# Kernel optimization log

Hardware: AMD Instinct MI355X
Metric: run time of the kernel (lower is better)

The kernel has to match this reference:

```python
import jax, jax.numpy as jnp
import numpy as np

B = 128
IN = 256
NLVL = 6
KLVL = 3
CH = 4
C = 4 * CH * CH          # 64 channels per node
OU = 8                   # out_filter_siz_u
OV = 8                   # out_filter_siz_v
NK = 2 ** KLVL           # 8 leaf nodes per axis
W_SCALE = 1.0 / 16.0     # ~1/sqrt(2*2*C) so 7 stacked relu-convs stay numerically sane


def setup_inputs() -> dict:
    key = jax.random.key(0)
    ks = jax.random.split(key, 2 * NLVL + 4)
    fx = IN // 2 ** NLVL  # 4: input patch filter size
    inp = {}
    inp["in_data"] = jax.random.normal(ks[0], (B, IN, IN, 1), jnp.float32)
    inp["in_filter"] = jax.random.normal(ks[1], (fx, fx, 1, C), jnp.float32) * W_SCALE
    inp["in_bias"] = jnp.zeros((C,), jnp.float32)
    i = 2
    for lvl in range(1, NLVL + 1):
        n = 2 ** min(lvl, KLVL)  # node grid: grows to 2^klvl then stays
        inp[f"f{lvl}"] = jax.random.normal(ks[i], (n, n, 2, 2, C, C), jnp.float32) * W_SCALE
        inp[f"b{lvl}"] = jnp.zeros((n, n, C), jnp.float32)
        i += 1
    inp["Wd"] = jax.random.normal(ks[i], (NK, NK, 2, C, OU * OV), jnp.float32) * W_SCALE
    return inp


def _node_conv(x, w, b):
    # x: [Nu,Nv,B,H,W,C]; w: [Nu,Nv,2,2,C,C]; 2x2 stride-2 VALID conv per node
    Nu, Nv, Bn, H, W, Cc = x.shape
    xr = x.reshape(Nu, Nv, Bn, H // 2, 2, W // 2, 2, Cc)
    y = jnp.einsum('uvbhxwyc,uvxyco->uvbhwo', xr, w)
    return jax.nn.relu(y + b[:, :, None, None, None, :])


def _forward(in_data, in_filter, in_bias, fs, bs, Wd):
    Bn = in_data.shape[0]
    fx, fy = in_filter.shape[0], in_filter.shape[1]
    # input interp conv: stride == kernel -> non-overlapping patch GEMM
    xr = in_data[..., 0].reshape(Bn, in_data.shape[1] // fx, fx, in_data.shape[2] // fy, fy)
    x = jax.nn.relu(jnp.einsum('bxpyq,pqc->bxyc', xr, in_filter[:, :, 0, :]) + in_bias)
    x = x[None, None]  # [1,1,B,2^nlvl,2^nlvl,C] node grid
    for lvl in range(1, NLVL + 1):
        if lvl <= KLVL:
            # children (itu,itv) read parent (itu//2, itv//2)
            x = jnp.repeat(jnp.repeat(x, 2, axis=0), 2, axis=1)
        x = _node_conv(x, fs[lvl - 1], bs[lvl - 1])
    feats = x[:, :, :, 0, 0, :]  # [NK,NK,B,C]; spatial is 1x1 at level nlvl
    out = jnp.einsum('uvbc,uvrck->uvbrk', feats, Wd)  # r in {real, imag}
    out = out.reshape(NK, NK, Bn, 2, OU, OV)
    out = jnp.transpose(out, (2, 0, 4, 1, 5, 3))  # [B,itu,ou,itv,ov,2]
    return out.reshape(Bn, NK * OU, NK * OV, 2)


def reference(in_data, in_filter, in_bias, f1, b1, f2, b2, f3, b3, f4, b4, f5, b5, f6, b6, Wd):
    fs = (f1, f2, f3, f4, f5, f6)
    bs = (b1, b2, b3, b4, b5, b6)
    return _forward(in_data, in_filter, in_bias, fs, bs, Wd)
```

## Files before the change

### kernel.cpp

```cpp
#include <hip/hip_runtime.h>
#include <hip/hip_bf16.h>
#include <cstdint>
#include <cstddef>


typedef __attribute__((ext_vector_type(8))) short short8;
typedef __attribute__((ext_vector_type(4))) float f32x4;
typedef unsigned short ushort_t;

static __device__ __forceinline__ float b2f(const __hip_bfloat16 x) {
    return __bfloat162float(x);
}
static __device__ __forceinline__ ushort_t f2bf(float x) {
    __hip_bfloat16 h = __float2bfloat16(x);
    ushort_t u;
    __builtin_memcpy(&u, &h, 2);
    return u;
}
static __device__ __forceinline__ void gl_lds16(const void* g, void* l) {
    __builtin_amdgcn_global_load_lds(
        (const __attribute__((address_space(1))) void*)g,
        (__attribute__((address_space(3))) void*)l, 16, 0, 0);
}
#define WAIT_LGKM0() __builtin_amdgcn_s_waitcnt(0xC07F)
#define WAIT_VM0()   __builtin_amdgcn_s_waitcnt(0x0F70)

#define PREP_BLOCKS 2533

static __device__ __forceinline__ void prep_work(
    int gid, int isbf,
    const void* f1, const void* f2, const void* f3,
    const void* f4, const void* f5, const void* f6, const void* wdsrc,
    const void* b1, const void* b2, const void* b3,
    const void* b4, const void* b5, const void* b6,
    ushort_t* __restrict__ wbuf, ushort_t* __restrict__ wdbuf,
    float* __restrict__ bbuf)
{
    if (gid >= 648448) return;
    if (gid >= 630784) {
        const int bg = gid - 630784;
        const void* src; int base;
        if      (bg <   256) { src = b1; base = 0;     }
        else if (bg <  1280) { src = b2; base = 256;   }
        else if (bg <  5376) { src = b3; base = 1280;  }
        else if (bg <  9472) { src = b4; base = 5376;  }
        else if (bg < 13568) { src = b5; base = 9472;  }
        else                 { src = b6; base = 13568; }
        const int local = bg - base;
        bbuf[bg] = isbf ? b2f(((const __hip_bfloat16*)src)[local])
                        : ((const float*)src)[local];
        return;
    }
    if (gid >= 565248) {
        const int local = gid - 565248;
        const int lane = local & 63;
        const int slot = (local >> 6) & 15;
        const int site = local >> 10;
        const int ks2 = slot >> 3, nh = slot & 7, q = lane >> 4;
        const int n = nh * 16 + (lane & 15);
        const int r = n >> 6, kk = n & 63;
        const int cbase = ks2 * 32 + q * 8;
        ushort_t pk[8];
        if (isbf) {
            const ushort_t* s = (const ushort_t*)wdsrc;
            #pragma unroll
            for (int j = 0; j < 8; j++)
                pk[j] = s[(((size_t)(site * 2 + r) * 64 + cbase + j) * 64) + kk];
        } else {
            const float* s = (const float*)wdsrc;
            #pragma unroll
            for (int j = 0; j < 8; j++)
                pk[j] = f2bf(s[(((size_t)(site * 2 + r) * 64 + cbase + j) * 64) + kk]);
        }
        *(uint4*)&wdbuf[(size_t)local * 8] = *(uint4*)pk;
        return;
    }
    const void* fsrc; int base;
    if      (gid <   8192) { fsrc = f1; base = 0;      }
    else if (gid <  40960) { fsrc = f2; base = 8192;   }
    else if (gid < 172032) { fsrc = f3; base = 40960;  }
    else if (gid < 303104) { fsrc = f4; base = 172032; }
    else if (gid < 434176) { fsrc = f5; base = 303104; }
    else                   { fsrc = f6; base = 434176; }
    const int local = gid - base;
    const int lane = local & 63;
    const int slot = (local >> 6) & 7;
    const int sitetap = local >> 9;
    const int ks = slot >> 2, nh = slot & 3, q = lane >> 4;
    const int n = (lane & 15) + nh * 16;
    const int kbase = ks * 32 + q * 8;
    ushort_t pk[8];
    if (isbf) {
        const ushort_t* s = (const ushort_t*)fsrc + (size_t)sitetap * 4096;
        #pragma unroll
        for (int j = 0; j < 8; j++) pk[j] = s[(kbase + j) * 64 + n];
    } else {
        const float* s = (const float*)fsrc + (size_t)sitetap * 4096;
        #pragma unroll
        for (int j = 0; j < 8; j++) pk[j] = f2bf(s[(kbase + j) * 64 + n]);
    }
    *(uint4*)&wbuf[(size_t)gid * 8] = *(uint4*)pk;
}

static __device__ __forceinline__ void stage0_body(
    int blk, int isbf,
    const void* __restrict__ in_data, const void* __restrict__ filt,
    const void* __restrict__ bias, __hip_bfloat16* __restrict__ x0,
    int b_off, int Bc)
{
    const int X  = blk & 63;
    const int bl = blk >> 6;
    const int bg = bl + b_off;

    __shared__ float sIn[4][256];
    __shared__ float sF[16][64];
    __shared__ float sB[64];

    const int t = threadIdx.x;
    const size_t srow = ((size_t)bg * 256 + (size_t)X * 4) * 256;

    if (isbf) {
        const __hip_bfloat16* src = (const __hip_bfloat16*)in_data + srow;
        #pragma unroll
        for (int i = 0; i < 4; i++) {
            int flat = i * 256 + t;
            int p = flat >> 8, col = flat & 255;
            sIn[p][col] = b2f(src[(size_t)p * 256 + col]);
        }
        const __hip_bfloat16* fsrc = (const __hip_bfloat16*)filt;
        #pragma unroll
        for (int i = 0; i < 4; i++) {
            int flat = i * 256 + t;
            sF[flat >> 6][flat & 63] = b2f(fsrc[flat]);
        }
        if (t < 64) sB[t] = b2f(((const __hip_bfloat16*)bias)[t]);
    } else {
        const float* src = (const float*)in_data + srow;
        const int p = t >> 6, c4 = (t & 63) * 4;
        *(float4*)&sIn[p][c4] = *(const float4*)(src + (size_t)p * 256 + c4);
        const float* fsrc = (const float*)filt;
        #pragma unroll
        for (int i = 0; i < 4; i++) {
            int flat = i * 256 + t;
            sF[flat >> 6][flat & 63] = fsrc[flat];
        }
        if (t < 64) sB[t] = ((const float*)bias)[t];
    }
    __syncthreads();

    const int ty = t >> 4;
    const int tc = t & 15;

    float acc[4][4];
    {
        const float4 bv = *(const float4*)&sB[tc * 4];
        #pragma unroll
        for (int yi = 0; yi < 4; yi++) {
            acc[yi][0] = bv.x; acc[yi][1] = bv.y;
            acc[yi][2] = bv.z; acc[yi][3] = bv.w;
        }
    }

    #pragma unroll
    for (int p = 0; p < 4; p++) {
        float4 rin[4], rf[4];
        #pragma unroll
        for (int yi = 0; yi < 4; yi++)
            rin[yi] = *(const float4*)&sIn[p][ty * 16 + yi * 4];
        #pragma unroll
        for (int q = 0; q < 4; q++)
            rf[q] = *(const float4*)&sF[p * 4 + q][tc * 4];
        #pragma unroll
        for (int yi = 0; yi < 4; yi++) {
            #pragma unroll
            for (int q = 0; q < 4; q++) {
                const float a = ((const float*)&rin[yi])[q];
                acc[yi][0] = fmaf(a, rf[q].x, acc[yi][0]);
                acc[yi][1] = fmaf(a, rf[q].y, acc[yi][1]);
                acc[yi][2] = fmaf(a, rf[q].z, acc[yi][2]);
                acc[yi][3] = fmaf(a, rf[q].w, acc[yi][3]);
            }
        }
    }

    ushort_t* dst = (ushort_t*)x0;
    #pragma unroll
    for (int yi = 0; yi < 4; yi++) {
        uint2 pk;
        pk.x = (uint32_t)f2bf(fmaxf(acc[yi][0], 0.f))
             | ((uint32_t)f2bf(fmaxf(acc[yi][1], 0.f)) << 16);
        pk.y = (uint32_t)f2bf(fmaxf(acc[yi][2], 0.f))
             | ((uint32_t)f2bf(fmaxf(acc[yi][3], 0.f)) << 16);
        const int wpos = ty * 4 + yi;
        *(uint2*)(dst + ((size_t)(X * 64 + wpos) * Bc + bl) * 64 + tc * 4) = pk;
    }
}

__global__ __launch_bounds__(256) void k_prep0(
    const void* __restrict__ in_data,
    const void* f1, const void* f2, const void* f3,
    const void* f4, const void* f5, const void* f6, const void* wdsrc,
    const void* b1, const void* b2, const void* b3,
    const void* b4, const void* b5, const void* b6,
    ushort_t* __restrict__ wbuf, ushort_t* __restrict__ wdbuf,
    float* __restrict__ bbuf, int* __restrict__ flag,
    const void* __restrict__ filt, const void* __restrict__ bias0,
    __hip_bfloat16* __restrict__ x0, int Bc)
{
    __shared__ int sflag;
    const int t = threadIdx.x;
    if (t < 64) {
        const float v = __uint_as_float(((const uint32_t*)in_data)[t]);
        const bool plaus = (v == 0.0f) || (fabsf(v) > 1e-8f && fabsf(v) < 1e4f);
        const unsigned long long m = __ballot(plaus);
        if (t == 0) sflag = (__popcll(m) >= 48) ? 0 : 1;
    }
    __syncthreads();
    const int isbf = sflag;

    if (blockIdx.x < PREP_BLOCKS) {
        if (blockIdx.x == 0 && t == 0) *flag = isbf;
        prep_work(blockIdx.x * 256 + t, isbf,
                  f1, f2, f3, f4, f5, f6, wdsrc,
                  b1, b2, b3, b4, b5, b6, wbuf, wdbuf, bbuf);
    } else {
        stage0_body(blockIdx.x - PREP_BLOCKS, isbf, in_data, filt, bias0, x0, 0, Bc);
    }
}

__global__ __launch_bounds__(256) void k_stage0(
    const void* __restrict__ in_data, const void* __restrict__ filt,
    const void* __restrict__ bias, __hip_bfloat16* __restrict__ x0,
    const int* __restrict__ flag, int b_off, int Bc)
{
    stage0_body(blockIdx.x, *flag, in_data, filt, bias, x0, b_off, Bc);
}

__global__ __launch_bounds__(256) void k_level4(
    const __hip_bfloat16* __restrict__ xin,
    const ushort_t* __restrict__ wbuf,
    const float* __restrict__ bbuf,
    __hip_bfloat16* __restrict__ xout,
    int Nv_out, int HW, int Bc, int mtiles)
{
    __shared__ ushort_t smem[20480];
    __shared__ float sBias[4][64];
    ushort_t* sA = smem;
    ushort_t* sB = smem + 4096;

    int idx = blockIdx.x;
    const int mt = idx % mtiles; idx /= mtiles;
    const int w  = idx % HW; idx /= HW;
    const int h  = idx % HW; idx /= HW;
    const int Nv_in = Nv_out >> 1;
    const int vp = idx % Nv_in;
    const int up = idx / Nv_in;

    const int t = threadIdx.x;
    const int wave = t >> 6, lane = t & 63;
    const int lm = lane & 15, lq = lane >> 4;

    {
        const int ct = t >> 6, o = t & 63;
        const int so_t = (2 * up + (ct >> 1)) * Nv_out + (2 * vp + (ct & 1));
        sBias[ct][o] = bbuf[so_t * 64 + o];
    }

    const int so = (2 * up + (wave >> 1)) * Nv_out + (2 * vp + (wave & 1));
    const int H_in = HW * 2;
    const size_t pstride = (size_t)Bc * 64;
    const size_t siteb = (size_t)(up * Nv_in + vp) * H_in * H_in * pstride;
    const ushort_t* wsite = wbuf + (size_t)so * 4 * 4096;

    const f32x4 zero = {0.f, 0.f, 0.f, 0.f};
    f32x4 acc[4][4];
    #pragma unroll
    for (int i = 0; i < 4; i++)
        #pragma unroll
        for (int j = 0; j < 4; j++) acc[i][j] = zero;

    for (int tap = 0; tap < 4; tap++) {
        const int hi = 2 * h + (tap >> 1), wi = 2 * w + (tap & 1);
        const size_t tapoff = siteb + ((size_t)hi * H_in + wi) * pstride;
        #pragma unroll
        for (int s2 = 0; s2 < 2; s2++) {
            const int s = wave * 2 + s2;
            const int ks = s >> 2, mh = s & 3;
            int b = mt * 64 + lm + mh * 16;
            if (b >= Bc) b = Bc - 1;
            gl_lds16(xin + tapoff + (size_t)b * 64 + ks * 32 + lq * 8,
                     &sA[s * 512]);
        }
        const ushort_t* wt = wsite + (size_t)tap * 4096;
        #pragma unroll
        for (int s = 0; s < 8; s++) {
            gl_lds16(wt + s * 512 + lane * 8, &sB[wave * 4096 + s * 512]);
        }
        __syncthreads();

        #pragma unroll
        for (int ks = 0; ks < 2; ks++) {
            short8 bf0 = *(const short8*)&sB[wave * 4096 + (ks * 4 + 0) * 512 + lane * 8];
            short8 bf1 = *(const short8*)&sB[wave * 4096 + (ks * 4 + 1) * 512 + lane * 8];
            short8 bf2 = *(const short8*)&sB[wave * 4096 + (ks * 4 + 2) * 512 + lane * 8];
            short8 bf3 = *(const short8*)&sB[wave * 4096 + (ks * 4 + 3) * 512 + lane * 8];
            #pragma unroll
            for (int fm = 0; fm < 4; fm++) {
                short8 a = *(const short8*)&sA[(ks * 4 + fm) * 512 + lane * 8];
                acc[fm][0] = __builtin_amdgcn_mfma_f32_16x16x32_bf16(a, bf0, acc[fm][0], 0, 0, 0);
                acc[fm][1] = __builtin_amdgcn_mfma_f32_16x16x32_bf16(a, bf1, acc[fm][1], 0, 0, 0);
                acc[fm][2] = __builtin_amdgcn_mfma_f32_16x16x32_bf16(a, bf2, acc[fm][2], 0, 0, 0);
                acc[fm][3] = __builtin_amdgcn_mfma_f32_16x16x32_bf16(a, bf3, acc[fm][3], 0, 0, 0);
            }
        }
        __syncthreads();
    }

    float bv[4];
    #pragma unroll
    for (int fn = 0; fn < 4; fn++) bv[fn] = sBias[wave][fn * 16 + lm];
    ushort_t* so_buf = smem + wave * 4352;
    #pragma unroll
    for (int fm = 0; fm < 4; fm++) {
        #pragma unroll
        for (int fn = 0; fn < 4; fn++) {
            #pragma unroll
            for (int r = 0; r < 4; r++) {
                const int row = fm * 16 + lq * 4 + r;
                so_buf[row * 68 + fn * 16 + lm] =
                    f2bf(fmaxf(acc[fm][fn][r] + bv[fn], 0.f));
            }
        }
    }
    __syncthreads();

    const size_t obase = ((size_t)so * HW * HW + (size_t)h * HW + w) * pstride;
    #pragma unroll
    for (int i = 0; i < 8; i++) {
        const int task = i * 64 + lane;
        const int oct = task & 7, row = task >> 3;
        const int b = mt * 64 + row;
        if (b < Bc) {
            *(uint4*)(xout + obase + (size_t)b * 64 + oct * 8) =
                *(const uint4*)&so_buf[row * 68 + oct * 8];
        }
    }
}

__global__ __launch_bounds__(256) void k_f456(
    const __hip_bfloat16* __restrict__ xin,
    const ushort_t* __restrict__ w4, const ushort_t* __restrict__ w5,
    const ushort_t* __restrict__ w6, const ushort_t* __restrict__ wd,
    const float* __restrict__ b4, const float* __restrict__ b5,
    const float* __restrict__ b6,
    void* __restrict__ out, const int* __restrict__ flag,
    int Bc, int b_off, int mtiles)
{
    const int isbf = *flag;
    const int bx = blockIdx.x;
    const int mt = bx % mtiles;
    const int site = bx / mtiles;
    const int u = site >> 3, v = site & 7;

    __shared__ ushort_t smem[37376];

    const int t = threadIdx.x;
    const int wv = t >> 6, lane = t & 63;
    const int lm = lane & 15, lq = lane >> 4;

    const ushort_t* w6s = w6 + (size_t)site * 16384 + lane * 8;
    const ushort_t* wds = wd + (size_t)site * 8192  + lane * 8;

    float bv4[4], bv5[4];
    #pragma unroll
    for (int fn = 0; fn < 4; fn++) {
        bv4[fn] = b4[site * 64 + fn * 16 + lm];
        bv5[fn] = b5[site * 64 + fn * 16 + lm];
    }
    const float bv6 = b6[site * 64 + wv * 16 + lm];

    {
        const ushort_t* w4s = w4 + (size_t)site * 16384;
        #pragma unroll
        for (int s2 = 0; s2 < 8; s2++) {
            const int s = wv * 8 + s2;
            gl_lds16(w4s + s * 512 + lane * 8, &smem[s * 512]);
        }
    }
    __syncthreads();

    const f32x4 zero = {0.f, 0.f, 0.f, 0.f};
    const int h5 = wv >> 1, w5p = wv & 1;
    ushort_t* mid1w = smem + 16384 + wv * 4224;
    ushort_t* Aw = smem + 33280 + wv * 1024;
    const size_t pstride = (size_t)Bc * 64;

    int brow = mt * 16 + lm;
    if (brow >= Bc) brow = Bc - 1;
    const __hip_bfloat16* xbase =
        xin + (size_t)site * 64 * pstride + (size_t)brow * 64 + lq * 8;

    for (int i = 0; i < 4; i++) {
        const int h4 = 2 * h5 + (i >> 1), w4p = 2 * w5p + (i & 1);
        f32x4 acc[4];
        #pragma unroll
        for (int b_ = 0; b_ < 4; b_++) acc[b_] = zero;

        for (int tap = 0; tap < 4; tap++) {
            const int h3 = 2 * h4 + (tap >> 1), w3 = 2 * w4p + (tap & 1);
            const size_t poff = (size_t)(h3 * 8 + w3) * pstride;
            WAIT_LGKM0();
            #pragma unroll
            for (int ks = 0; ks < 2; ks++) {
                gl_lds16(xbase + poff + ks * 32, &Aw[ks * 512]);
            }
            WAIT_VM0();
            __builtin_amdgcn_sched_barrier(0);
            #pragma unroll
            for (int ks = 0; ks < 2; ks++) {
                short8 a = *(const short8*)&Aw[ks * 512 + lane * 8];
                #pragma unroll
                for (int fn = 0; fn < 4; fn++) {
                    short8 bfr = *(const short8*)&smem[(tap * 8 + ks * 4 + fn) * 512 + lane * 8];
                    acc[fn] = __builtin_amdgcn_mfma_f32_16x16x32_bf16(a, bfr, acc[fn], 0, 0, 0);
                }
            }
        }
        #pragma unroll
        for (int fn = 0; fn < 4; fn++) {
            #pragma unroll
            for (int r = 0; r < 4; r++) {
                const int m = lq * 4 + r;
                const int ch = fn * 16 + lm;
                mid1w[m * 264 + i * 64 + ch] =
                    f2bf(fmaxf(acc[fn][r] + bv4[fn], 0.f));
            }
        }
    }
    __syncthreads();

    {
        const ushort_t* w5s = w5 + (size_t)site * 16384;
        #pragma unroll
        for (int s2 = 0; s2 < 8; s2++) {
            const int s = wv * 8 + s2;
            gl_lds16(w5s + s * 512 + lane * 8, &smem[s * 512]);
        }
    }
    __syncthreads();

    short8 b3r[8];
    short8 wdr[4];
    {
        f32x4 acc2[4];
        #pragma unroll
        for (int b_ = 0; b_ < 4; b_++) acc2[b_] = zero;

        #pragma unroll
        for (int i = 0; i < 4; i++) {
            #pragma unroll
            for (int ks = 0; ks < 2; ks++) {
                short8 a0 = *(const short8*)&mid1w[lm * 264 + i * 64 + ks * 32 + lq * 8];
                #pragma unroll
                for (int fn = 0; fn < 4; fn++) {
                    short8 bfr = *(const short8*)&smem[(i * 8 + ks * 4 + fn) * 512 + lane * 8];
                    acc2[fn] = __builtin_amdgcn_mfma_f32_16x16x32_bf16(a0, bfr, acc2[fn], 0, 0, 0);
                }
            }
        }

        #pragma unroll
        for (int tap = 0; tap < 4; tap++)
            #pragma unroll
            for (int ks = 0; ks < 2; ks++)
                b3r[tap * 2 + ks] = *(const short8*)(w6s + (tap * 8 + ks * 4 + wv) * 512);
        #pragma unroll
        for (int ks = 0; ks < 2; ks++)
            #pragma unroll
            for (int n2 = 0; n2 < 2; n2++)
                wdr[ks * 2 + n2] = *(const short8*)(wds + (ks * 8 + 2 * wv + n2) * 512);

        #pragma unroll
        for (int fn = 0; fn < 4; fn++) {
            #pragma unroll
            for (int r = 0; r < 4; r++) {
                const int m = lq * 4 + r;
                const int ch = fn * 16 + lm;
                mid1w[m * 72 + ch] =
                    f2bf(fmaxf(acc2[fn][r] + bv5[fn], 0.f));
            }
        }
    }
    __syncthreads();

    {
        f32x4 acc3 = zero;
        #pragma unroll
        for (int tap = 0; tap < 4; tap++) {
            const ushort_t* sl = smem + 16384 + tap * 4224;
            #pragma unroll
            for (int ks = 0; ks < 2; ks++) {
                short8 a0 = *(const short8*)&sl[lm * 72 + ks * 32 + lq * 8];
                acc3 = __builtin_amdgcn_mfma_f32_16x16x32_bf16(a0, b3r[tap * 2 + ks], acc3, 0, 0, 0);
            }
        }
        ushort_t* mid3 = smem + 33280;
        #pragma unroll
        for (int r = 0; r < 4; r++) {
            const int m = lq * 4 + r;
            const int ch = wv * 16 + lm;
            mid3[m * 72 + ch] = f2bf(fmaxf(acc3[r] + bv6, 0.f));
        }
    }
    __syncthreads();

    {
        const ushort_t* mid3 = smem + 33280;
        f32x4 acc4[2];
        acc4[0] = zero; acc4[1] = zero;
        #pragma unroll
        for (int ks = 0; ks < 2; ks++) {
            short8 a0 = *(const short8*)&mid3[lm * 72 + ks * 32 + lq * 8];
            #pragma unroll
            for (int n2 = 0; n2 < 2; n2++) {
                acc4[n2] = __builtin_amdgcn_mfma_f32_16x16x32_bf16(a0, wdr[ks * 2 + n2], acc4[n2], 0, 0, 0);
            }
        }
        #pragma unroll
        for (int n2 = 0; n2 < 2; n2++) {
            const int n = (2 * wv + n2) * 16 + lm;
            const int rr = n >> 6, ou = (n >> 3) & 7, ov = n & 7;
            const size_t obase =
                (((size_t)(u * 8 + ou)) * 64 + (v * 8 + ov)) * 2 + rr;
            #pragma unroll
            for (int reg = 0; reg < 4; reg++) {
                const int brw = mt * 16 + lq * 4 + reg;
                if (brw < Bc) {
                    const size_t oidx = obase + (size_t)(b_off + brw) * 8192;
                    if (isbf) ((__hip_bfloat16*)out)[oidx] =
                        __float2bfloat16(acc4[n2][reg]);
                    else ((float*)out)[oidx] = acc4[n2][reg];
                }
            }
        }
    }
}

extern "C" void kernel_launch(void* const* d_in, const int* in_sizes, int n_in,
                              void* d_out, int out_size, void* d_ws, size_t ws_size,
                              hipStream_t stream)
{
    (void)in_sizes; (void)n_in; (void)out_size;

    const void* in_data = d_in[0];
    const void* filt    = d_in[1];
    const void* bias0   = d_in[2];
    const void* fl[7];
    const void* bl[7];
    for (int l = 1; l <= 6; l++) {
        fl[l] = d_in[1 + 2 * l];
        bl[l] = d_in[2 + 2 * l];
    }
    const void* Wd = d_in[15];

    const int Bfull = 128;
    const size_t perB = (size_t)64 * 64 * 64;

    const size_t wbufBytes  = 565248ull * 16;
    const size_t wdbufBytes = 65536ull * 16;
    const size_t bbufBytes  = 17664ull * 4;
    const size_t headBytes  = 256 + wbufBytes + wdbufBytes + bbufBytes;

    const size_t avail = ws_size > headBytes ? ws_size - headBytes : 0;
    int Bc = 0;
    for (int c = 128; c >= 1; c >>= 1) {
        if ((size_t)2 * c * perB * sizeof(__hip_bfloat16) <= avail) { Bc = c; break; }
    }
    if (Bc == 0) return;

    int* flag = (int*)d_ws;
    ushort_t* wbuf  = (ushort_t*)((char*)d_ws + 256);
    ushort_t* wdbuf = (ushort_t*)((char*)d_ws + 256 + wbufBytes);
    float* bbuf = (float*)((char*)d_ws + 256 + wbufBytes + wdbufBytes);
    __hip_bfloat16* bufA = (__hip_bfloat16*)((char*)d_ws + headBytes);
    __hip_bfloat16* bufB = bufA + (size_t)Bc * perB;

    static const size_t w_off[7] = {0, 0, 65536, 327680, 1376256, 2424832, 3473408};
    static const int    b_off_tab[7] = {0, 0, 256, 1280, 5376, 9472, 13568};

    const int mt4 = (Bc + 63) / 64;
    const int mt16 = (Bc + 15) / 16;

    for (int b_off = 0; b_off < Bfull; b_off += Bc) {
        if (b_off == 0) {
            k_prep0<<<dim3(PREP_BLOCKS + Bc * 64), 256, 0, stream>>>(
                in_data,
                fl[1], fl[2], fl[3], fl[4], fl[5], fl[6], Wd,
                bl[1], bl[2], bl[3], bl[4], bl[5], bl[6],
                wbuf, wdbuf, bbuf, flag,
                filt, bias0, bufA, Bc);
        } else {
            k_stage0<<<dim3(Bc * 64), 256, 0, stream>>>(in_data, filt, bias0, bufA, flag, b_off, Bc);
        }

        __hip_bfloat16* cur = bufA;
        __hip_bfloat16* nxt = bufB;
        for (int lvl = 1; lvl <= 3; lvl++) {
            const int Nu = 1 << lvl;
            const int H  = 64 >> lvl;
            const int Nv_in = Nu >> 1;
            dim3 grid(Nv_in * Nv_in * H * H * mt4);
            k_level4<<<grid, 256, 0, stream>>>(cur, wbuf + w_off[lvl],
                bbuf + b_off_tab[lvl], nxt, Nu, H, Bc, mt4);
            __hip_bfloat16* tmp = cur; cur = nxt; nxt = tmp;
        }

        k_f456<<<dim3(64 * mt16), 256, 0, stream>>>(cur,
            wbuf + w_off[4], wbuf + w_off[5], wbuf + w_off[6], wdbuf,
            bbuf + b_off_tab[4], bbuf + b_off_tab[5], bbuf + b_off_tab[6],
            d_out, flag, Bc, b_off, mt16);
    }
}
```

Measured before the change: 249.0 us.

## Prefetch all level-4 taps at once and hold weights in registers

The level-4 node-conv kernel now issues every activation load for all four taps to LDS up front, one tap per wave, instead of running a load/sync/compute loop per tap. Each wave's weights (32 short8 fragments) go straight from global memory into registers, skipping the LDS weight staging and the bias shared-memory table. This cuts the per-tap barriers and the serialised load latency, and it shrinks LDS use, with a launch bound of 2 blocks per CU. In exchange it needs many more vector registers (128 VGPRs for weights plus accumulators), which could force spills or lower occupancy.

```diff
diff --git a/kernel.cpp b/kernel.cpp
--- a/kernel.cpp
+++ b/kernel.cpp
@@ -236,17 +236,14 @@
     stage0_body(blockIdx.x, *flag, in_data, filt, bias, x0, b_off, Bc);
 }
 
-__global__ __launch_bounds__(256) void k_level4(
+__global__ __launch_bounds__(256, 2) void k_level4(
     const __hip_bfloat16* __restrict__ xin,
     const ushort_t* __restrict__ wbuf,
     const float* __restrict__ bbuf,
     __hip_bfloat16* __restrict__ xout,
     int Nv_out, int HW, int Bc, int mtiles)
 {
-    __shared__ ushort_t smem[20480];
-    __shared__ float sBias[4][64];
-    ushort_t* sA = smem;
-    ushort_t* sB = smem + 4096;
+    __shared__ ushort_t smem[17408];
 
     int idx = blockIdx.x;
     const int mt = idx % mtiles; idx /= mtiles;
@@ -260,17 +257,35 @@
     const int wave = t >> 6, lane = t & 63;
     const int lm = lane & 15, lq = lane >> 4;
 
-    {
-        const int ct = t >> 6, o = t & 63;
-        const int so_t = (2 * up + (ct >> 1)) * Nv_out + (2 * vp + (ct & 1));
-        sBias[ct][o] = bbuf[so_t * 64 + o];
-    }
-
     const int so = (2 * up + (wave >> 1)) * Nv_out + (2 * vp + (wave & 1));
     const int H_in = HW * 2;
     const size_t pstride = (size_t)Bc * 64;
     const size_t siteb = (size_t)(up * Nv_in + vp) * H_in * H_in * pstride;
-    const ushort_t* wsite = wbuf + (size_t)so * 4 * 4096;
+    const ushort_t* wsite = wbuf + (size_t)so * 4 * 4096 + lane * 8;
+
+    {
+        const int hi = 2 * h + (wave >> 1), wi = 2 * w + (wave & 1);
+        const size_t tapoff = siteb + ((size_t)hi * H_in + wi) * pstride;
+        #pragma unroll
+        for (int j = 0; j < 8; j++) {
+            const int ks = j >> 2, mh = j & 3;
+            int b = mt * 64 + mh * 16 + lm;
+            if (b >= Bc) b = Bc - 1;
+            gl_lds16(xin + tapoff + (size_t)b * 64 + ks * 32 + lq * 8,
+                     &smem[(wave * 8 + j) * 512]);
+        }
+    }
+
+    short8 breg[32];
+    #pragma unroll
+    for (int s = 0; s < 32; s++)
+        breg[s] = *(const short8*)(wsite + s * 512);
+
+    float bv[4];
+    #pragma unroll
+    for (int fn = 0; fn < 4; fn++) bv[fn] = bbuf[so * 64 + fn * 16 + lm];
+
+    __syncthreads();
 
     const f32x4 zero = {0.f, 0.f, 0.f, 0.f};
     f32x4 acc[4][4];
@@ -279,46 +294,22 @@
         #pragma unroll
         for (int j = 0; j < 4; j++) acc[i][j] = zero;
 
+    #pragma unroll
     for (int tap = 0; tap < 4; tap++) {
-        const int hi = 2 * h + (tap >> 1), wi = 2 * w + (tap & 1);
-        const size_t tapoff = siteb + ((size_t)hi * H_in + wi) * pstride;
-        #pragma unroll
-        for (int s2 = 0; s2 < 2; s2++) {
-            const int s = wave * 2 + s2;
-            const int ks = s >> 2, mh = s & 3;
-            int b = mt * 64 + lm + mh * 16;
-            if (b >= Bc) b = Bc - 1;
-            gl_lds16(xin + tapoff + (size_t)b * 64 + ks * 32 + lq * 8,
-                     &sA[s * 512]);
-        }
-        const ushort_t* wt = wsite + (size_t)tap * 4096;
-        #pragma unroll
-        for (int s = 0; s < 8; s++) {
-            gl_lds16(wt + s * 512 + lane * 8, &sB[wave * 4096 + s * 512]);
-        }
-        __syncthreads();
-
         #pragma unroll
         for (int ks = 0; ks < 2; ks++) {
-            short8 bf0 = *(const short8*)&sB[wave * 4096 + (ks * 4 + 0) * 512 + lane * 8];
-            short8 bf1 = *(const short8*)&sB[wave * 4096 + (ks * 4 + 1) * 512 + lane * 8];
-            short8 bf2 = *(const short8*)&sB[wave * 4096 + (ks * 4 + 2) * 512 + lane * 8];
-            short8 bf3 = *(const short8*)&sB[wave * 4096 + (ks * 4 + 3) * 512 + lane * 8];
             #pragma unroll
             for (int fm = 0; fm < 4; fm++) {
-                short8 a = *(const short8*)&sA[(ks * 4 + fm) * 512 + lane * 8];
-                acc[fm][0] = __builtin_amdgcn_mfma_f32_16x16x32_bf16(a, bf0, acc[fm][0], 0, 0, 0);
-                acc[fm][1] = __builtin_amdgcn_mfma_f32_16x16x32_bf16(a, bf1, acc[fm][1], 0, 0, 0);
-                acc[fm][2] = __builtin_amdgcn_mfma_f32_16x16x32_bf16(a, bf2, acc[fm][2], 0, 0, 0);
-                acc[fm][3] = __builtin_amdgcn_mfma_f32_16x16x32_bf16(a, bf3, acc[fm][3], 0, 0, 0);
-            }
-        }
-        __syncthreads();
-    }
-
-    float bv[4];
-    #pragma unroll
-    for (int fn = 0; fn < 4; fn++) bv[fn] = sBias[wave][fn * 16 + lm];
+                short8 a = *(const short8*)&smem[(tap * 8 + ks * 4 + fm) * 512 + lane * 8];
+                #pragma unroll
+                for (int fn = 0; fn < 4; fn++)
+                    acc[fm][fn] = __builtin_amdgcn_mfma_f32_16x16x32_bf16(
+                        a, breg[tap * 8 + ks * 4 + fn], acc[fm][fn], 0, 0, 0);
+            }
+        }
+    }
+    __syncthreads();
+
     ushort_t* so_buf = smem + wave * 4352;
     #pragma unroll
     for (int fm = 0; fm < 4; fm++) {
```

After: 249.2 us. Within noise of the previous version (+0.1%).
